# Performance work log

Hardware: AMD Instinct MI355X
Metric: run time of the kernel (lower is better)

Reference implementation:

```python
import jax, jax.numpy as jnp
import numpy as np

# ---- configuration mirrored from init_kwargs ----
NUM_TREES = 8
NUM_NODES = 5
C = 16          # in_channels
B, H, W = 8, 224, 224
SEED = 0
NEG = -1e30     # maxplus semiring zero (avoid -inf for fp16/bf16 safety)


def make_forest():
    """Random recursive trees: node 0 is the root, parent[i] < i."""
    rng = np.random.default_rng(SEED)
    parents = []
    for _ in range(NUM_TREES):
        p = [-1] + [int(rng.integers(0, i)) for i in range(1, NUM_NODES)]
        parents.append(p)
    return parents


def excl_prefix_max(v):
    """Strict 2D prefix max: out[h,w] = max over h'<h, w'<w of v[h',w'].
    Semiring 'cumulative sum' (maxplus add = max) with exclusive shift."""
    c = jax.lax.cummax(jax.lax.cummax(v, axis=2), axis=3)
    c = c[:, :, :-1, :-1]
    return jnp.pad(c, ((0, 0), (0, 0), (1, 0), (1, 0)), constant_values=NEG)


def setup_inputs() -> dict:
    key = jax.random.key(0)
    kx, ka = jax.random.split(key)
    x = jax.random.normal(kx, (B, C, H, W), dtype=jnp.float32)
    alphas = jax.random.normal(ka, (NUM_TREES, NUM_NODES, C), dtype=jnp.float32)
    return {"x": x, "alphas": alphas}


def reference(x, alphas):
    parents = make_forest()  # static structure (seed-fixed)
    # valuate: map to log domain for the maxplus semiring
    xv = jnp.log1p(jax.nn.relu(x))  # [B, C, H, W]

    outs = []
    for t in range(NUM_TREES):
        par = parents[t]
        acc = [None] * NUM_NODES   # maxplus-product (= +) of children prefix maxes
        root_val = None
        # bottom-up over nodes (parent index < child index)
        for i in range(NUM_NODES - 1, -1, -1):
            # maxplus scaling by alpha: alpha + x
            v = xv + alphas[t, i][None, :, None, None]
            if acc[i] is not None:
                v = v + acc[i]          # semiring product with children
            if i > 0:
                s = excl_prefix_max(v)  # semiring cumulative over quadrant
                p = par[i]
                acc[p] = s if acc[p] is None else acc[p] + s
            else:
                root_val = v
        # root aggregation: maxplus sum over all pixels -> [B, C]
        outs.append(jnp.max(root_val, axis=(2, 3)))
    res = jnp.stack(outs, axis=1)  # [B, NUM_TREES, C]
    # devaluate: back from log domain
    return jnp.expm1(res)
```

## Files before the change

kernel.cpp:

```cpp
#include <hip/hip_runtime.h>
#include <stdint.h>

#define NTREES 8
#define NNODES 5
#define CC 16
#define BB 8
#define HH 224
#define WW 224

struct Forest { int par[NTREES * NNODES]; };
struct Cls { int v[NTREES]; };

namespace nprng {

struct Pcg {
  __uint128_t state, inc;
  int has_uint32;
  uint32_t uinteger;
};

static inline __uint128_t pcg_mult() {
  return (((__uint128_t)0x2360ED051FC65DA4ULL) << 64) | 0x4385DF649FCCF645ULL;
}

static inline void pcg_step(Pcg& s) { s.state = s.state * pcg_mult() + s.inc; }

static inline uint64_t pcg_next64(Pcg& s) {
  pcg_step(s);
  uint64_t xored = (uint64_t)(s.state >> 64) ^ (uint64_t)s.state;
  unsigned rot = (unsigned)(s.state >> 122);
  return (xored >> rot) | (xored << ((64u - rot) & 63u));
}

static inline uint32_t pcg_next32(Pcg& s) {
  if (s.has_uint32) { s.has_uint32 = 0; return s.uinteger; }
  uint64_t n = pcg_next64(s);
  s.has_uint32 = 1;
  s.uinteger = (uint32_t)(n >> 32);
  return (uint32_t)n;
}

static inline uint32_t lemire32(Pcg& s, uint32_t rng) {
  const uint32_t rng_excl = rng + 1u;
  uint64_t m = (uint64_t)pcg_next32(s) * (uint64_t)rng_excl;
  uint32_t leftover = (uint32_t)m;
  if (leftover < rng_excl) {
    const uint32_t threshold = (uint32_t)((0xFFFFFFFFu - rng) % rng_excl);
    while (leftover < threshold) {
      m = (uint64_t)pcg_next32(s) * (uint64_t)rng_excl;
      leftover = (uint32_t)m;
    }
  }
  return (uint32_t)(m >> 32);
}

static void make_forest(Forest& f) {
  const uint32_t INIT_A = 0x43b0d7e5u, MULT_A = 0x931e8875u;
  const uint32_t INIT_B = 0x8b51f9ddu, MULT_B = 0x58f38dedu;
  const uint32_t MIX_L  = 0xca01f9ddu, MIX_R  = 0x4973f715u;
  uint32_t pool[4];
  uint32_t hc = INIT_A;
  auto hashmix = [&](uint32_t v) -> uint32_t {
    v ^= hc; hc *= MULT_A; v *= hc; v ^= v >> 16; return v;
  };
  auto mix = [&](uint32_t x, uint32_t y) -> uint32_t {
    uint32_t r = MIX_L * x - MIX_R * y; r ^= r >> 16; return r;
  };
  pool[0] = hashmix(0u);
  for (int i = 1; i < 4; ++i) pool[i] = hashmix(0u);
  for (int is = 0; is < 4; ++is)
    for (int id = 0; id < 4; ++id)
      if (is != id) pool[id] = mix(pool[id], hashmix(pool[is]));
  uint32_t st32[8];
  uint32_t hb = INIT_B;
  for (int i = 0; i < 8; ++i) {
    uint32_t dv = pool[i & 3];
    dv ^= hb; hb *= MULT_B; dv *= hb; dv ^= dv >> 16;
    st32[i] = dv;
  }
  uint64_t w64[4];
  for (int i = 0; i < 4; ++i)
    w64[i] = (uint64_t)st32[2 * i] | ((uint64_t)st32[2 * i + 1] << 32);

  __uint128_t initstate = (((__uint128_t)w64[0]) << 64) | w64[1];
  __uint128_t initseq   = (((__uint128_t)w64[2]) << 64) | w64[3];
  Pcg s;
  s.state = 0; s.inc = (initseq << 1) | 1;
  pcg_step(s);
  s.state += initstate;
  pcg_step(s);
  s.has_uint32 = 0; s.uinteger = 0;

  for (int t = 0; t < NTREES; ++t) {
    f.par[t * NNODES + 0] = -1;
    for (int i = 1; i < NNODES; ++i) {
      uint32_t rng = (uint32_t)(i - 1);
      f.par[t * NNODES + i] = (rng == 0) ? 0 : (int)lemire32(s, rng);
    }
  }
}

}

static int classify_tree(const int* p) {
  int nch[NNODES] = {0, 0, 0, 0, 0};
  for (int i = 1; i < NNODES; ++i) nch[p[i]]++;
  int internals[3], nI = 0;
  for (int i = 1; i <= 3; ++i) if (nch[i] > 0) internals[nI++] = i;
  if (nI == 0) return 1;
  if (nI == 1) {
    int m = nch[internals[0]];
    return m == 1 ? 2 : (m == 2 ? 3 : 4);
  }
  if (nI == 2) {
    int i = internals[0], j = internals[1];
    if (p[j] == i) {
      if (nch[j] == 2) return 9;
      return (nch[i] - 1 == 1) ? 7 : 6;
    }
    return 5;
  }
  return 8;
}

template <int C> struct Cfg;
template <> struct Cfg<1> { static constexpr int NE=0,E1L=0,E2L=0,E2E1=0,RL=4,RE1=0,RE2=0,RE3=0; };
template <> struct Cfg<2> { static constexpr int NE=1,E1L=1,E2L=0,E2E1=0,RL=2,RE1=1,RE2=0,RE3=0; };
template <> struct Cfg<3> { static constexpr int NE=1,E1L=2,E2L=0,E2E1=0,RL=1,RE1=1,RE2=0,RE3=0; };
template <> struct Cfg<4> { static constexpr int NE=1,E1L=3,E2L=0,E2E1=0,RL=0,RE1=1,RE2=0,RE3=0; };
template <> struct Cfg<5> { static constexpr int NE=1,E1L=1,E2L=0,E2E1=0,RL=0,RE1=2,RE2=0,RE3=0; };
template <> struct Cfg<6> { static constexpr int NE=2,E1L=1,E2L=0,E2E1=1,RL=1,RE1=0,RE2=1,RE3=0; };
template <> struct Cfg<7> { static constexpr int NE=2,E1L=1,E2L=1,E2E1=1,RL=0,RE1=0,RE2=1,RE3=0; };
template <> struct Cfg<8> { static constexpr int NE=3,E1L=1,E2L=0,E2E1=1,RL=0,RE1=0,RE2=0,RE3=1; };
template <> struct Cfg<9> { static constexpr int NE=2,E1L=2,E2L=0,E2E1=1,RL=0,RE1=0,RE2=1,RE3=0; };

__device__ __forceinline__ float wshr1(float t) {
  int r = __builtin_amdgcn_update_dpp(
      0, __builtin_bit_cast(int, t), 0x138, 0xf, 0xf, true);
  return __builtin_bit_cast(float, r);
}

#define SCAN_OP(Q, MODS) \
  asm volatile("v_max_f32_dpp %0, %0, %0 " MODS : "+v"(Q))

#define STAGE(MODS)                                         \
  {                                                         \
    SCAN_OP(q[0], MODS);                                    \
    if constexpr (K > 1) SCAN_OP(q[1], MODS);               \
    if constexpr (K > 2) SCAN_OP(q[2], MODS);               \
    if constexpr (K > 3) SCAN_OP(q[3], MODS);               \
    if constexpr (K == 1) asm volatile("s_nop 1");          \
    else if constexpr (K == 2) asm volatile("s_nop 0");     \
  }

#define FENCE_ALL()                                                             \
  {                                                                             \
    if constexpr (K == 1) asm volatile("s_nop 1" : "+v"(q[0]));                 \
    else if constexpr (K == 2)                                                  \
      asm volatile("s_nop 1" : "+v"(q[0]), "+v"(q[1]));                         \
    else if constexpr (K == 3)                                                  \
      asm volatile("s_nop 1" : "+v"(q[0]), "+v"(q[1]), "+v"(q[2]));             \
    else                                                                        \
      asm volatile("s_nop 1" : "+v"(q[0]), "+v"(q[1]), "+v"(q[2]), "+v"(q[3])); \
  }

#define MUL4(d, s) { (d).x *= (s).x; (d).y *= (s).y; (d).z *= (s).z; (d).w *= (s).w; }
#define MAX4(d, s) { (d).x = fmaxf((d).x,(s).x); (d).y = fmaxf((d).y,(s).y); \
                     (d).z = fmaxf((d).z,(s).z); (d).w = fmaxf((d).w,(s).w); }

template <int E>
__device__ __forceinline__ void powmul(float4& v, const float4& s) {
  if constexpr (E == 4) {
    float4 t = s; MUL4(t, t); MUL4(t, t); MUL4(v, t);
  } else {
    if constexpr (E >= 1) MUL4(v, s);
    if constexpr (E >= 2) MUL4(v, s);
    if constexpr (E >= 3) MUL4(v, s);
  }
}

template <int CLS>
__device__ __forceinline__ void run_tree(const float* __restrict__ cp,
                                         float mask, float asum,
                                         float* __restrict__ outp, int lane) {
  using C = Cfg<CLS>;
  constexpr int K = 1 + C::NE;

  const float4 zero4 = make_float4(0.f, 0.f, 0.f, 0.f);
  float4 pm[4] = {zero4, zero4, zero4, zero4};
  float4 racc = zero4;

  auto row_step = [&](const float4& xr) {
    float4 fv;
    fv.x = fmaf(fmaxf(xr.x, 0.f), mask, mask);
    fv.y = fmaf(fmaxf(xr.y, 0.f), mask, mask);
    fv.z = fmaf(fmaxf(xr.z, 0.f), mask, mask);
    fv.w = fmaf(fmaxf(xr.w, 0.f), mask, mask);

    float4 s[4];
#pragma unroll
    for (int k = 0; k < K; ++k)
      s[k] = make_float4(wshr1(pm[k].w), pm[k].x, pm[k].y, pm[k].z);

    float4 v0 = fv;
    powmul<C::RL>(v0, s[0]);
    if constexpr (C::RE1 > 0) powmul<C::RE1>(v0, s[1]);
    if constexpr (C::RE2 > 0) powmul<C::RE2>(v0, s[2]);
    if constexpr (C::RE3 > 0) powmul<C::RE3>(v0, s[3]);
    MAX4(racc, v0);

    float4 vv[4];
    vv[0] = fv;
    if constexpr (C::NE >= 1) { vv[1] = fv; powmul<C::E1L>(vv[1], s[0]); }
    if constexpr (C::NE >= 2) {
      vv[2] = fv; powmul<C::E2L>(vv[2], s[0]); powmul<C::E2E1>(vv[2], s[1]);
    }
    if constexpr (C::NE >= 3) { vv[3] = fv; powmul<1>(vv[3], s[2]); }

    float l0[4], l1[4], l2[4], q[4];
#pragma unroll
    for (int k = 0; k < K; ++k) {
      l0[k] = vv[k].x;
      l1[k] = fmaxf(l0[k], vv[k].y);
      l2[k] = fmaxf(l1[k], vv[k].z);
      q[k]  = fmaxf(l2[k], vv[k].w);
    }

    FENCE_ALL();
    STAGE("row_shr:1 row_mask:0xf bank_mask:0xf");
    STAGE("row_shr:2 row_mask:0xf bank_mask:0xf");
    STAGE("row_shr:4 row_mask:0xf bank_mask:0xf");
    STAGE("row_shr:8 row_mask:0xf bank_mask:0xf");
    STAGE("row_bcast:15 row_mask:0xa bank_mask:0xf");
    STAGE("row_bcast:31 row_mask:0xc bank_mask:0xf");
    FENCE_ALL();

#pragma unroll
    for (int k = 0; k < K; ++k) {
      float e = wshr1(q[k]);
      pm[k].x = fmaxf(fmaxf(e, l0[k]), pm[k].x);
      pm[k].y = fmaxf(fmaxf(e, l1[k]), pm[k].y);
      pm[k].z = fmaxf(fmaxf(e, l2[k]), pm[k].z);
      pm[k].w = fmaxf(q[k], pm[k].w);
    }
  };

  float4 A0 = *(const float4*)(cp + 0 * WW);
  float4 A1 = *(const float4*)(cp + 1 * WW);
  float4 A2 = *(const float4*)(cp + 2 * WW);
  float4 A3 = *(const float4*)(cp + 3 * WW);
  float4 B0 = *(const float4*)(cp + 4 * WW);
  float4 B1 = *(const float4*)(cp + 5 * WW);
  float4 B2 = *(const float4*)(cp + 6 * WW);
  float4 B3 = *(const float4*)(cp + 7 * WW);

#pragma unroll 2
  for (int h = 0; h < HH; h += 4) {
    const int n0 = (h +  8 < HH) ? h +  8 : HH - 1;
    const int n1 = (h +  9 < HH) ? h +  9 : HH - 1;
    const int n2 = (h + 10 < HH) ? h + 10 : HH - 1;
    const int n3 = (h + 11 < HH) ? h + 11 : HH - 1;
    float4 T0 = *(const float4*)(cp + (size_t)n0 * WW);
    float4 T1 = *(const float4*)(cp + (size_t)n1 * WW);
    float4 T2 = *(const float4*)(cp + (size_t)n2 * WW);
    float4 T3 = *(const float4*)(cp + (size_t)n3 * WW);

    row_step(A0);
    row_step(A1);
    row_step(A2);
    row_step(A3);

    A0 = B0; A1 = B1; A2 = B2; A3 = B3;
    B0 = T0; B1 = T1; B2 = T2; B3 = T3;
  }

  float m = fmaxf(fmaxf(racc.x, racc.y), fmaxf(racc.z, racc.w));
#pragma unroll
  for (int d = 1; d < 64; d <<= 1) m = fmaxf(m, __shfl_xor(m, d));
  if (lane == 0) *outp = expf(asum) * m - 1.0f;
}

__global__ __launch_bounds__(64) void fis_kernel(const float* __restrict__ x,
                                                 const float* __restrict__ alphas,
                                                 float* __restrict__ out,
                                                 Cls cls) {
  const int lane = threadIdx.x;
  const int blk  = blockIdx.x;
  const int t    = blk >> 7;
  const int bc   = blk & 127;
  const int c    = bc & (CC - 1);
  const int b    = bc >> 4;

  const float* __restrict__ xp = x + (size_t)bc * (HH * WW);

  float asum = 0.f;
#pragma unroll
  for (int i = 0; i < NNODES; ++i) asum += alphas[(t * NNODES + i) * CC + c];

  const int   w0   = lane * 4;
  const float mask = (w0 < WW) ? 1.0f : 0.0f;
  const float* __restrict__ cp = xp + ((w0 < WW) ? w0 : (WW - 4));
  float* outp = out + ((size_t)b * NTREES + t) * CC + c;

  switch (cls.v[t]) {
    case 1: run_tree<1>(cp, mask, asum, outp, lane); break;
    case 2: run_tree<2>(cp, mask, asum, outp, lane); break;
    case 3: run_tree<3>(cp, mask, asum, outp, lane); break;
    case 4: run_tree<4>(cp, mask, asum, outp, lane); break;
    case 5: run_tree<5>(cp, mask, asum, outp, lane); break;
    case 6: run_tree<6>(cp, mask, asum, outp, lane); break;
    case 7: run_tree<7>(cp, mask, asum, outp, lane); break;
    case 8: run_tree<8>(cp, mask, asum, outp, lane); break;
    case 9: run_tree<9>(cp, mask, asum, outp, lane); break;
    default: break;
  }
}

extern "C" void kernel_launch(void* const* d_in, const int* in_sizes, int n_in,
                              void* d_out, int out_size, void* d_ws, size_t ws_size,
                              hipStream_t stream) {
  const float* x      = (const float*)d_in[0];
  const float* alphas = (const float*)d_in[1];
  float* out          = (float*)d_out;

  Forest f;
  nprng::make_forest(f);

  Cls cls;
  for (int t = 0; t < NTREES; ++t)
    cls.v[t] = classify_tree(&f.par[t * NNODES]);

  dim3 grid(BB * CC * NTREES);
  dim3 block(64);
  hipLaunchKernelGGL(fis_kernel, grid, block, 0, stream, x, alphas, out, cls);
}
```

Measured before the change: 100.2 us.

## Process rows in bands of eight with batched DPP scans per tree level

The row loop now works on bands of 8 rows. Instead of doing one scan per row across all tree levels, it runs one 8-wide batched DPP scan per tree level, carrying prefix state between rows inside the band. The aim is to fill DPP hazard slots with independent rows, cut the s_nop overhead, and give more instruction-level parallelism than the row-serial chain did. The cost is higher register pressure from the per-band M arrays and a full-band prefetch of 8 rows, which may lower occupancy or cause spills.

```diff
diff --git a/kernel.cpp b/kernel.cpp
--- a/kernel.cpp
+++ b/kernel.cpp
@@ -7,6 +7,7 @@
 #define BB 8
 #define HH 224
 #define WW 224
+#define NBAND 28
 
 struct Forest { int par[NTREES * NNODES]; };
 struct Cls { int v[NTREES]; };
@@ -123,16 +124,16 @@
   return 8;
 }
 
-template <int C> struct Cfg;
-template <> struct Cfg<1> { static constexpr int NE=0,E1L=0,E2L=0,E2E1=0,RL=4,RE1=0,RE2=0,RE3=0; };
-template <> struct Cfg<2> { static constexpr int NE=1,E1L=1,E2L=0,E2E1=0,RL=2,RE1=1,RE2=0,RE3=0; };
-template <> struct Cfg<3> { static constexpr int NE=1,E1L=2,E2L=0,E2E1=0,RL=1,RE1=1,RE2=0,RE3=0; };
-template <> struct Cfg<4> { static constexpr int NE=1,E1L=3,E2L=0,E2E1=0,RL=0,RE1=1,RE2=0,RE3=0; };
-template <> struct Cfg<5> { static constexpr int NE=1,E1L=1,E2L=0,E2E1=0,RL=0,RE1=2,RE2=0,RE3=0; };
-template <> struct Cfg<6> { static constexpr int NE=2,E1L=1,E2L=0,E2E1=1,RL=1,RE1=0,RE2=1,RE3=0; };
-template <> struct Cfg<7> { static constexpr int NE=2,E1L=1,E2L=1,E2E1=1,RL=0,RE1=0,RE2=1,RE3=0; };
-template <> struct Cfg<8> { static constexpr int NE=3,E1L=1,E2L=0,E2E1=1,RL=0,RE1=0,RE2=0,RE3=1; };
-template <> struct Cfg<9> { static constexpr int NE=2,E1L=2,E2L=0,E2E1=1,RL=0,RE1=0,RE2=1,RE3=0; };
+template <int CL> struct TC;
+template <> struct TC<1> { static constexpr int H1=0,E1L=0,H2=0,E2L=0,H3=0,RL=4,R1=0,R2=0,R3=0; };
+template <> struct TC<2> { static constexpr int H1=1,E1L=1,H2=0,E2L=0,H3=0,RL=2,R1=1,R2=0,R3=0; };
+template <> struct TC<3> { static constexpr int H1=1,E1L=2,H2=0,E2L=0,H3=0,RL=1,R1=1,R2=0,R3=0; };
+template <> struct TC<4> { static constexpr int H1=1,E1L=3,H2=0,E2L=0,H3=0,RL=0,R1=1,R2=0,R3=0; };
+template <> struct TC<5> { static constexpr int H1=1,E1L=1,H2=0,E2L=0,H3=0,RL=0,R1=2,R2=0,R3=0; };
+template <> struct TC<6> { static constexpr int H1=1,E1L=1,H2=1,E2L=0,H3=0,RL=1,R1=0,R2=1,R3=0; };
+template <> struct TC<7> { static constexpr int H1=1,E1L=1,H2=1,E2L=1,H3=0,RL=0,R1=0,R2=1,R3=0; };
+template <> struct TC<8> { static constexpr int H1=1,E1L=1,H2=1,E2L=0,H3=1,RL=0,R1=0,R2=0,R3=1; };
+template <> struct TC<9> { static constexpr int H1=1,E1L=2,H2=1,E2L=0,H3=0,RL=0,R1=0,R2=1,R3=0; };
 
 __device__ __forceinline__ float wshr1(float t) {
   int r = __builtin_amdgcn_update_dpp(
@@ -140,29 +141,28 @@
   return __builtin_bit_cast(float, r);
 }
 
-#define SCAN_OP(Q, MODS) \
-  asm volatile("v_max_f32_dpp %0, %0, %0 " MODS : "+v"(Q))
-
-#define STAGE(MODS)                                         \
-  {                                                         \
-    SCAN_OP(q[0], MODS);                                    \
-    if constexpr (K > 1) SCAN_OP(q[1], MODS);               \
-    if constexpr (K > 2) SCAN_OP(q[2], MODS);               \
-    if constexpr (K > 3) SCAN_OP(q[3], MODS);               \
-    if constexpr (K == 1) asm volatile("s_nop 1");          \
-    else if constexpr (K == 2) asm volatile("s_nop 0");     \
-  }
-
-#define FENCE_ALL()                                                             \
-  {                                                                             \
-    if constexpr (K == 1) asm volatile("s_nop 1" : "+v"(q[0]));                 \
-    else if constexpr (K == 2)                                                  \
-      asm volatile("s_nop 1" : "+v"(q[0]), "+v"(q[1]));                         \
-    else if constexpr (K == 3)                                                  \
-      asm volatile("s_nop 1" : "+v"(q[0]), "+v"(q[1]), "+v"(q[2]));             \
-    else                                                                        \
-      asm volatile("s_nop 1" : "+v"(q[0]), "+v"(q[1]), "+v"(q[2]), "+v"(q[3])); \
-  }
+#define S8STAGE(MODS) \
+  "v_max_f32_dpp %0, %0, %0 " MODS "\n\t" \
+  "v_max_f32_dpp %1, %1, %1 " MODS "\n\t" \
+  "v_max_f32_dpp %2, %2, %2 " MODS "\n\t" \
+  "v_max_f32_dpp %3, %3, %3 " MODS "\n\t" \
+  "v_max_f32_dpp %4, %4, %4 " MODS "\n\t" \
+  "v_max_f32_dpp %5, %5, %5 " MODS "\n\t" \
+  "v_max_f32_dpp %6, %6, %6 " MODS "\n\t" \
+  "v_max_f32_dpp %7, %7, %7 " MODS "\n\t"
+
+#define SCAN8(q)                                              \
+  asm volatile(                                               \
+      "s_nop 1\n\t"                                           \
+      S8STAGE("row_shr:1 row_mask:0xf bank_mask:0xf")         \
+      S8STAGE("row_shr:2 row_mask:0xf bank_mask:0xf")         \
+      S8STAGE("row_shr:4 row_mask:0xf bank_mask:0xf")         \
+      S8STAGE("row_shr:8 row_mask:0xf bank_mask:0xf")         \
+      S8STAGE("row_bcast:15 row_mask:0xa bank_mask:0xf")      \
+      S8STAGE("row_bcast:31 row_mask:0xc bank_mask:0xf")      \
+      "s_nop 1"                                               \
+      : "+v"(q[0]), "+v"(q[1]), "+v"(q[2]), "+v"(q[3]),       \
+        "+v"(q[4]), "+v"(q[5]), "+v"(q[6]), "+v"(q[7]))
 
 #define MUL4(d, s) { (d).x *= (s).x; (d).y *= (s).y; (d).z *= (s).z; (d).w *= (s).w; }
 #define MAX4(d, s) { (d).x = fmaxf((d).x,(s).x); (d).y = fmaxf((d).y,(s).y); \
@@ -179,105 +179,161 @@
   }
 }
 
-template <int CLS>
+__device__ __forceinline__ float4 shiftrow(const float4* M, int u, const float4& carry) {
+  float4 p = (u == 0) ? carry : M[u - 1];
+  return make_float4(wshr1(p.w), p.x, p.y, p.z);
+}
+
+template <int CL>
 __device__ __forceinline__ void run_tree(const float* __restrict__ cp,
                                          float mask, float asum,
                                          float* __restrict__ outp, int lane) {
-  using C = Cfg<CLS>;
-  constexpr int K = 1 + C::NE;
-
-  const float4 zero4 = make_float4(0.f, 0.f, 0.f, 0.f);
-  float4 pm[4] = {zero4, zero4, zero4, zero4};
-  float4 racc = zero4;
-
-  auto row_step = [&](const float4& xr) {
-    float4 fv;
-    fv.x = fmaf(fmaxf(xr.x, 0.f), mask, mask);
-    fv.y = fmaf(fmaxf(xr.y, 0.f), mask, mask);
-    fv.z = fmaf(fmaxf(xr.z, 0.f), mask, mask);
-    fv.w = fmaf(fmaxf(xr.w, 0.f), mask, mask);
-
-    float4 s[4];
-#pragma unroll
-    for (int k = 0; k < K; ++k)
-      s[k] = make_float4(wshr1(pm[k].w), pm[k].x, pm[k].y, pm[k].z);
-
-    float4 v0 = fv;
-    powmul<C::RL>(v0, s[0]);
-    if constexpr (C::RE1 > 0) powmul<C::RE1>(v0, s[1]);
-    if constexpr (C::RE2 > 0) powmul<C::RE2>(v0, s[2]);
-    if constexpr (C::RE3 > 0) powmul<C::RE3>(v0, s[3]);
-    MAX4(racc, v0);
-
-    float4 vv[4];
-    vv[0] = fv;
-    if constexpr (C::NE >= 1) { vv[1] = fv; powmul<C::E1L>(vv[1], s[0]); }
-    if constexpr (C::NE >= 2) {
-      vv[2] = fv; powmul<C::E2L>(vv[2], s[0]); powmul<C::E2E1>(vv[2], s[1]);
-    }
-    if constexpr (C::NE >= 3) { vv[3] = fv; powmul<1>(vv[3], s[2]); }
-
-    float l0[4], l1[4], l2[4], q[4];
-#pragma unroll
-    for (int k = 0; k < K; ++k) {
-      l0[k] = vv[k].x;
-      l1[k] = fmaxf(l0[k], vv[k].y);
-      l2[k] = fmaxf(l1[k], vv[k].z);
-      q[k]  = fmaxf(l2[k], vv[k].w);
-    }
-
-    FENCE_ALL();
-    STAGE("row_shr:1 row_mask:0xf bank_mask:0xf");
-    STAGE("row_shr:2 row_mask:0xf bank_mask:0xf");
-    STAGE("row_shr:4 row_mask:0xf bank_mask:0xf");
-    STAGE("row_shr:8 row_mask:0xf bank_mask:0xf");
-    STAGE("row_bcast:15 row_mask:0xa bank_mask:0xf");
-    STAGE("row_bcast:31 row_mask:0xc bank_mask:0xf");
-    FENCE_ALL();
-
-#pragma unroll
-    for (int k = 0; k < K; ++k) {
-      float e = wshr1(q[k]);
-      pm[k].x = fmaxf(fmaxf(e, l0[k]), pm[k].x);
-      pm[k].y = fmaxf(fmaxf(e, l1[k]), pm[k].y);
-      pm[k].z = fmaxf(fmaxf(e, l2[k]), pm[k].z);
-      pm[k].w = fmaxf(q[k], pm[k].w);
-    }
-  };
-
-  float4 A0 = *(const float4*)(cp + 0 * WW);
-  float4 A1 = *(const float4*)(cp + 1 * WW);
-  float4 A2 = *(const float4*)(cp + 2 * WW);
-  float4 A3 = *(const float4*)(cp + 3 * WW);
-  float4 B0 = *(const float4*)(cp + 4 * WW);
-  float4 B1 = *(const float4*)(cp + 5 * WW);
-  float4 B2 = *(const float4*)(cp + 6 * WW);
-  float4 B3 = *(const float4*)(cp + 7 * WW);
-
-#pragma unroll 2
-  for (int h = 0; h < HH; h += 4) {
-    const int n0 = (h +  8 < HH) ? h +  8 : HH - 1;
-    const int n1 = (h +  9 < HH) ? h +  9 : HH - 1;
-    const int n2 = (h + 10 < HH) ? h + 10 : HH - 1;
-    const int n3 = (h + 11 < HH) ? h + 11 : HH - 1;
-    float4 T0 = *(const float4*)(cp + (size_t)n0 * WW);
-    float4 T1 = *(const float4*)(cp + (size_t)n1 * WW);
-    float4 T2 = *(const float4*)(cp + (size_t)n2 * WW);
-    float4 T3 = *(const float4*)(cp + (size_t)n3 * WW);
-
-    row_step(A0);
-    row_step(A1);
-    row_step(A2);
-    row_step(A3);
-
-    A0 = B0; A1 = B1; A2 = B2; A3 = B3;
-    B0 = T0; B1 = T1; B2 = T2; B3 = T3;
+  using F = TC<CL>;
+  const float4 z4 = make_float4(0.f, 0.f, 0.f, 0.f);
+  float4 cL = z4, c1 = z4, c2 = z4, c3 = z4, racc = z4;
+
+  float4 X[8];
+#pragma unroll
+  for (int u = 0; u < 8; ++u) X[u] = *(const float4*)(cp + u * WW);
+
+#pragma unroll 1
+  for (int band = 0; band < NBAND; ++band) {
+    const int nb = (band + 1 < NBAND) ? band + 1 : NBAND - 1;
+    float4 T[8];
+#pragma unroll
+    for (int u = 0; u < 8; ++u)
+      T[u] = *(const float4*)(cp + (size_t)(nb * 8 + u) * WW);
+
+    float4 fv[8];
+#pragma unroll
+    for (int u = 0; u < 8; ++u) {
+      const float4 xr = X[u];
+      fv[u].x = fmaf(fmaxf(xr.x, 0.f), mask, mask);
+      fv[u].y = fmaf(fmaxf(xr.y, 0.f), mask, mask);
+      fv[u].z = fmaf(fmaxf(xr.z, 0.f), mask, mask);
+      fv[u].w = fmaf(fmaxf(xr.w, 0.f), mask, mask);
+    }
+
+    float4 ML[8], M1[8], M2[8], M3[8];
+
+    {
+      float l0[8], l1[8], l2[8], q[8];
+#pragma unroll
+      for (int u = 0; u < 8; ++u) {
+        l0[u] = fv[u].x;
+        l1[u] = fmaxf(l0[u], fv[u].y);
+        l2[u] = fmaxf(l1[u], fv[u].z);
+        q[u]  = fmaxf(l2[u], fv[u].w);
+      }
+      SCAN8(q);
+      float4 run = cL;
+#pragma unroll
+      for (int u = 0; u < 8; ++u) {
+        float e = wshr1(q[u]);
+        run.x = fmaxf(run.x, fmaxf(e, l0[u]));
+        run.y = fmaxf(run.y, fmaxf(e, l1[u]));
+        run.z = fmaxf(run.z, fmaxf(e, l2[u]));
+        run.w = fmaxf(run.w, q[u]);
+        ML[u] = run;
+      }
+    }
+
+    if constexpr (F::H1) {
+      float l0[8], l1[8], l2[8], q[8];
+#pragma unroll
+      for (int u = 0; u < 8; ++u) {
+        float4 v = fv[u];
+        powmul<F::E1L>(v, shiftrow(ML, u, cL));
+        l0[u] = v.x;
+        l1[u] = fmaxf(l0[u], v.y);
+        l2[u] = fmaxf(l1[u], v.z);
+        q[u]  = fmaxf(l2[u], v.w);
+      }
+      SCAN8(q);
+      float4 run = c1;
+#pragma unroll
+      for (int u = 0; u < 8; ++u) {
+        float e = wshr1(q[u]);
+        run.x = fmaxf(run.x, fmaxf(e, l0[u]));
+        run.y = fmaxf(run.y, fmaxf(e, l1[u]));
+        run.z = fmaxf(run.z, fmaxf(e, l2[u]));
+        run.w = fmaxf(run.w, q[u]);
+        M1[u] = run;
+      }
+    }
+
+    if constexpr (F::H2) {
+      float l0[8], l1[8], l2[8], q[8];
+#pragma unroll
+      for (int u = 0; u < 8; ++u) {
+        float4 v = fv[u];
+        if constexpr (F::E2L > 0) powmul<F::E2L>(v, shiftrow(ML, u, cL));
+        { float4 s1 = shiftrow(M1, u, c1); MUL4(v, s1); }
+        l0[u] = v.x;
+        l1[u] = fmaxf(l0[u], v.y);
+        l2[u] = fmaxf(l1[u], v.z);
+        q[u]  = fmaxf(l2[u], v.w);
+      }
+      SCAN8(q);
+      float4 run = c2;
+#pragma unroll
+      for (int u = 0; u < 8; ++u) {
+        float e = wshr1(q[u]);
+        run.x = fmaxf(run.x, fmaxf(e, l0[u]));
+        run.y = fmaxf(run.y, fmaxf(e, l1[u]));
+        run.z = fmaxf(run.z, fmaxf(e, l2[u]));
+        run.w = fmaxf(run.w, q[u]);
+        M2[u] = run;
+      }
+    }
+
+    if constexpr (F::H3) {
+      float l0[8], l1[8], l2[8], q[8];
+#pragma unroll
+      for (int u = 0; u < 8; ++u) {
+        float4 v = fv[u];
+        { float4 s2 = shiftrow(M2, u, c2); MUL4(v, s2); }
+        l0[u] = v.x;
+        l1[u] = fmaxf(l0[u], v.y);
+        l2[u] = fmaxf(l1[u], v.z);
+        q[u]  = fmaxf(l2[u], v.w);
+      }
+      SCAN8(q);
+      float4 run = c3;
+#pragma unroll
+      for (int u = 0; u < 8; ++u) {
+        float e = wshr1(q[u]);
+        run.x = fmaxf(run.x, fmaxf(e, l0[u]));
+        run.y = fmaxf(run.y, fmaxf(e, l1[u]));
+        run.z = fmaxf(run.z, fmaxf(e, l2[u]));
+        run.w = fmaxf(run.w, q[u]);
+        M3[u] = run;
+      }
+    }
+
+#pragma unroll
+    for (int u = 0; u < 8; ++u) {
+      float4 r = fv[u];
+      if constexpr (F::RL > 0) powmul<F::RL>(r, shiftrow(ML, u, cL));
+      if constexpr (F::R1 > 0) powmul<F::R1>(r, shiftrow(M1, u, c1));
+      if constexpr (F::R2 > 0) powmul<F::R2>(r, shiftrow(M2, u, c2));
+      if constexpr (F::R3 > 0) powmul<F::R3>(r, shiftrow(M3, u, c3));
+      MAX4(racc, r);
+    }
+
+    cL = ML[7];
+    if constexpr (F::H1) c1 = M1[7];
+    if constexpr (F::H2) c2 = M2[7];
+    if constexpr (F::H3) c3 = M3[7];
+
+#pragma unroll
+    for (int u = 0; u < 8; ++u) X[u] = T[u];
   }
 
   float m = fmaxf(fmaxf(racc.x, racc.y), fmaxf(racc.z, racc.w));
 #pragma unroll
   for (int d = 1; d < 64; d <<= 1) m = fmaxf(m, __shfl_xor(m, d));
-  if (lane == 0) *outp = expf(asum) * m - 1.0f;
+  if (lane == 0) *outp = expf(asum) * m - 1.f;
 }
 
 __global__ __launch_bounds__(64) void fis_kernel(const float* __restrict__ x,
```

New measurement: 98.31 us. No clear change (-1.9%).
